# Optimization experiments

Hardware: AMD Instinct MI355X
Metric: run time of the kernel (lower is better)

The kernel has to match this reference:

```python
import jax, jax.numpy as jnp
import numpy as np

D_MODEL = 1024
N_HEADS = 16
HEAD_DIM = D_MODEL // N_HEADS
SEQ_LEN = 2048
BATCH = 4


def setup_inputs() -> dict:
    key = jax.random.key(0)
    k1, k2, k3 = jax.random.split(key, 3)
    x = jax.random.normal(k1, (BATCH, SEQ_LEN, D_MODEL), dtype=jnp.float32)
    # Linear weights stored as [in, out] so y = x @ W (equivalent to torch x @ W.T)
    w_qkv = jax.random.normal(k2, (D_MODEL, 3 * D_MODEL), dtype=jnp.float32) * (D_MODEL ** -0.5)
    w_proj = jax.random.normal(k3, (D_MODEL, D_MODEL), dtype=jnp.float32) * (D_MODEL ** -0.5)
    return {"x": x, "w_qkv": w_qkv, "w_proj": w_proj}


def reference(x, w_qkv, w_proj):
    B, T, C = x.shape
    qkv = x @ w_qkv  # [B, T, 3C]
    q, k, v = jnp.split(qkv, 3, axis=-1)
    # [B, H, T, hd]
    q = q.reshape(B, T, N_HEADS, HEAD_DIM).transpose(0, 2, 1, 3)
    k = k.reshape(B, T, N_HEADS, HEAD_DIM).transpose(0, 2, 1, 3)
    v = v.reshape(B, T, N_HEADS, HEAD_DIM).transpose(0, 2, 1, 3)
    scale = HEAD_DIM ** -0.5
    attn = jnp.einsum("bhqd,bhkd->bhqk", q, k) * scale  # [B, H, T, T]
    causal = jnp.tril(jnp.ones((T, T), dtype=bool))
    attn = jnp.where(causal, attn, -jnp.inf)
    attn = jax.nn.softmax(attn, axis=-1)
    out = jnp.einsum("bhqk,bhkd->bhqd", attn, v)  # [B, H, T, hd]
    out = out.transpose(0, 2, 1, 3).reshape(B, T, C)
    return out @ w_proj
```

## Files before the change

### kernel.cpp

```cpp
#include <hip/hip_runtime.h>
#include <stdint.h>


typedef __bf16 bf16x8 __attribute__((ext_vector_type(8)));
typedef float f32x4 __attribute__((ext_vector_type(4)));
typedef unsigned short u16x8 __attribute__((ext_vector_type(8)));

#define DEVINL static __device__ __forceinline__

DEVINL unsigned short f2b(float f) {
  __bf16 h = (__bf16)f;
  return __builtin_bit_cast(unsigned short, h);
}

DEVINL void gld16(const void* g, void* l) {
  __builtin_amdgcn_global_load_lds(
      (const __attribute__((address_space(1))) void*)g,
      (__attribute__((address_space(3))) void*)l, 16, 0, 0);
}

DEVINL f32x4 mfma16(bf16x8 a, bf16x8 b, f32x4 c) {
  return __builtin_amdgcn_mfma_f32_16x16x32_bf16(a, b, c, 0, 0, 0);
}

#define SCHED_FENCE() __builtin_amdgcn_sched_barrier(0)

__global__ __launch_bounds__(256) void k_cast_bf16(const float* __restrict__ in,
                                                   unsigned short* __restrict__ out,
                                                   int n8) {
  int i = blockIdx.x * 256 + threadIdx.x;
  if (i >= n8) return;
  const float4* p = (const float4*)in + (size_t)i * 2;
  float4 a = p[0], b = p[1];
  u16x8 o;
  o[0] = f2b(a.x); o[1] = f2b(a.y); o[2] = f2b(a.z); o[3] = f2b(a.w);
  o[4] = f2b(b.x); o[5] = f2b(b.y); o[6] = f2b(b.z); o[7] = f2b(b.w);
  *(u16x8*)(out + (size_t)i * 8) = o;
}

__global__ __launch_bounds__(256) void k_transpose_w(const float* __restrict__ in,
                                                     unsigned short* __restrict__ out,
                                                     int R, int C) {
  __shared__ float t[64][65];
  int ci = blockIdx.x * 64, ri = blockIdx.y * 64;
  int tid = threadIdx.x;
#pragma unroll
  for (int j = 0; j < 4; ++j) {
    int c = tid + j * 256;
    int row = c >> 4;
    int col = (c & 15) * 4;
    float4 v = *(const float4*)(in + (size_t)(ri + row) * C + ci + col);
    t[row][col] = v.x; t[row][col + 1] = v.y; t[row][col + 2] = v.z; t[row][col + 3] = v.w;
  }
  __syncthreads();
  int cc = tid >> 2;
  int seg = (tid & 3) * 16;
  u16x8 o0, o1;
#pragma unroll
  for (int j = 0; j < 8; ++j) o0[j] = f2b(t[seg + j][cc]);
#pragma unroll
  for (int j = 0; j < 8; ++j) o1[j] = f2b(t[seg + 8 + j][cc]);
  unsigned short* dst = out + (size_t)(ci + cc) * R + ri + seg;
  *(u16x8*)dst = o0;
  *(u16x8*)(dst + 8) = o1;
}

__global__ __launch_bounds__(256) void k_transpose_v(const unsigned short* __restrict__ v,
                                                     unsigned short* __restrict__ vt) {
  __shared__ unsigned short s[64][65];
  int bh = blockIdx.y;
  int t0 = blockIdx.x * 64;
  int tid = threadIdx.x;
  const unsigned short* src = v + ((size_t)bh * 2048 + t0) * 64;
#pragma unroll
  for (int j = 0; j < 2; ++j) {
    int c = tid + j * 256;
    int row = c >> 3;
    int col = (c & 7) * 8;
    u16x8 x = *(const u16x8*)(src + (size_t)row * 64 + col);
#pragma unroll
    for (int q = 0; q < 8; ++q) s[row][col + q] = x[q];
  }
  __syncthreads();
  int d = tid >> 2;
  int seg = (tid & 3) * 16;
  u16x8 o0, o1;
#pragma unroll
  for (int j = 0; j < 8; ++j) o0[j] = s[seg + j][d];
#pragma unroll
  for (int j = 0; j < 8; ++j) o1[j] = s[seg + 8 + j][d];
  unsigned short* dst = vt + ((size_t)bh * 64 + d) * 2048 + t0 + seg;
  *(u16x8*)dst = o0;
  *(u16x8*)(dst + 8) = o1;
}

template <int MODE>
__global__ __launch_bounds__(256) void k_gemm(const unsigned short* __restrict__ A,
                                              const unsigned short* __restrict__ Bt,
                                              int M, int N, int K,
                                              float* __restrict__ Cf,
                                              unsigned short* __restrict__ qo,
                                              unsigned short* __restrict__ ko,
                                              unsigned short* __restrict__ vo,
                                              float qscale) {
  __shared__ unsigned short As[128 * 32];
  __shared__ unsigned short Bs[128 * 32];
  int tid = threadIdx.x;
  int w = tid >> 6, lane = tid & 63, l15 = lane & 15, l4 = lane >> 4;
  int bn = blockIdx.x, bm = blockIdx.y;
  int wr = (w >> 1) * 64, wc = (w & 1) * 64;
  f32x4 acc[4][4];
#pragma unroll
  for (int i = 0; i < 4; ++i)
#pragma unroll
    for (int j = 0; j < 4; ++j) acc[i][j] = (f32x4){0.f, 0.f, 0.f, 0.f};
  const char* Ab = (const char*)(A + (size_t)bm * 128 * K);
  const char* Bb = (const char*)(Bt + (size_t)bn * 128 * K);
  for (int kt = 0; kt < K; kt += 32) {
#pragma unroll
    for (int c0 = 0; c0 < 2; ++c0) {
      int c = tid + c0 * 256;
      int row = c >> 2, cb = (c & 3) * 16;
      gld16(Ab + ((size_t)row * K + kt) * 2 + cb, (char*)As + c * 16);
      gld16(Bb + ((size_t)row * K + kt) * 2 + cb, (char*)Bs + c * 16);
    }
    __syncthreads();
    bf16x8 af[4], bfr[4];
#pragma unroll
    for (int m = 0; m < 4; ++m)
      af[m] = *(const bf16x8*)((const char*)As + (wr + m * 16 + l15) * 64 + l4 * 16);
#pragma unroll
    for (int n = 0; n < 4; ++n)
      bfr[n] = *(const bf16x8*)((const char*)Bs + (wc + n * 16 + l15) * 64 + l4 * 16);
#pragma unroll
    for (int m = 0; m < 4; ++m)
#pragma unroll
      for (int n = 0; n < 4; ++n)
        acc[m][n] = mfma16(af[m], bfr[n], acc[m][n]);
    __syncthreads();
  }
#pragma unroll
  for (int m = 0; m < 4; ++m) {
    int grow0 = bm * 128 + wr + m * 16 + l4 * 4;
#pragma unroll
    for (int n = 0; n < 4; ++n) {
      int gcol = bn * 128 + wc + n * 16 + l15;
#pragma unroll
      for (int r = 0; r < 4; ++r) {
        int grow = grow0 + r;
        float val = acc[m][n][r];
        if (MODE == 1) {
          Cf[(size_t)grow * N + gcol] = val;
        } else {
          int which = gcol >> 10, rem = gcol & 1023;
          int h = rem >> 6, d = rem & 63;
          int b = grow >> 11, t = grow & 2047;
          size_t off = (((size_t)(b * 16 + h)) * 2048 + t) * 64 + d;
          if (which == 0)      qo[off] = f2b(val * qscale);
          else if (which == 1) ko[off] = f2b(val);
          else                 vo[off] = f2b(val);
        }
      }
    }
  }
}

__global__ __launch_bounds__(256) void k_attn(const unsigned short* __restrict__ Q,
                                              const unsigned short* __restrict__ Kt,
                                              const unsigned short* __restrict__ Vt,
                                              unsigned short* __restrict__ AO) {
  __shared__ unsigned short Ks[2][4096];
  __shared__ unsigned short Vs[2][4096];
  __shared__ unsigned short Ps[4096];
  int tid = threadIdx.x;
  int w = tid >> 6, lane = tid & 63, l15 = lane & 15, l4 = lane >> 4;
  int lin = blockIdx.x;
  int xcd = lin & 7, jj = lin >> 3;
  int bh = xcd * 8 + (jj & 7);
  int p = jj >> 3;
  const char* Kb = (const char*)(Kt + (size_t)bh * 2048 * 64);
  const char* Vb = (const char*)(Vt + (size_t)bh * 64 * 2048);
  const int swp = (l15 & 7) << 4;
  char* Pw = (char*)Ps + w * 2048;
  int b = bh >> 4, h = bh & 15;

  int Lb0 = (w * 64 + lane) * 16;
  int Lb1 = ((w + 4) * 64 + lane) * 16;
  int Nb0 = Lb0 ^ (((Lb0 >> 7) & 7) << 4);
  int Nb1 = Lb1 ^ (((Lb1 >> 7) & 7) << 4);
  int d0 = Nb0 >> 7, in0 = Nb0 & 127;
  int d1 = Nb1 >> 7, in1 = Nb1 & 127;

  auto stage = [&](int t, int buf) {
    size_t kv0 = (size_t)t * 64;
    gld16(Kb + kv0 * 128 + Nb0, (char*)Ks[buf] + Lb0);
    gld16(Vb + (size_t)d0 * 4096 + kv0 * 2 + in0, (char*)Vs[buf] + Lb0);
    gld16(Kb + kv0 * 128 + Nb1, (char*)Ks[buf] + Lb1);
    gld16(Vb + (size_t)d1 * 4096 + kv0 * 2 + in1, (char*)Vs[buf] + Lb1);
  };

  auto run = [&](int qi) {
    int q0 = qi * 64;
    const unsigned short* Qb = Q + ((size_t)bh * 2048 + q0 + w * 16) * 64;
    bf16x8 qf0 = *(const bf16x8*)((const char*)Qb + l15 * 128 + l4 * 16);
    bf16x8 qf1 = *(const bf16x8*)((const char*)Qb + l15 * 128 + 64 + l4 * 16);
    f32x4 o[4];
#pragma unroll
    for (int i = 0; i < 4; ++i) o[i] = (f32x4){0.f, 0.f, 0.f, 0.f};
    float mrow = -1e30f, lrow = 0.f;
    const int ntiles = qi + 1;
    const int qg = w * 16 + l15;
    SCHED_FENCE();
    __builtin_amdgcn_s_barrier();
    SCHED_FENCE();
    stage(0, 0);
    SCHED_FENCE();
    for (int it = 0; it < ntiles; ++it) {
      int cur = it & 1;
      if (it) {
        SCHED_FENCE();
        __builtin_amdgcn_s_barrier();
        SCHED_FENCE();
      }
      if (it + 1 < ntiles) {
        stage(it + 1, cur ^ 1);
        SCHED_FENCE();
        asm volatile("s_waitcnt vmcnt(4)" ::: "memory");
      } else {
        SCHED_FENCE();
        asm volatile("s_waitcnt vmcnt(0)" ::: "memory");
      }
      SCHED_FENCE();
      __builtin_amdgcn_s_barrier();
      SCHED_FENCE();
      const char* Kc = (const char*)Ks[cur];
      const char* Vc = (const char*)Vs[cur];
      f32x4 s[4];
      __builtin_amdgcn_s_setprio(1);
#pragma unroll
      for (int c = 0; c < 4; ++c) {
        int row = c * 16 + l15;
        int base = row * 128 + l4 * 16;
        int sw = (row & 7) << 4;
        bf16x8 k0 = *(const bf16x8*)(Kc + (base ^ sw));
        bf16x8 k1 = *(const bf16x8*)(Kc + ((base + 64) ^ sw));
        f32x4 t = mfma16(k0, qf0, (f32x4){0.f, 0.f, 0.f, 0.f});
        s[c] = mfma16(k1, qf1, t);
      }
      __builtin_amdgcn_s_setprio(0);
      if (it == ntiles - 1) {
#pragma unroll
        for (int c = 0; c < 4; ++c) {
          int kvb = c * 16 + l4 * 4;
#pragma unroll
          for (int r = 0; r < 4; ++r)
            if (kvb + r > qg) s[c][r] = -1e30f;
        }
      }
      float mx = fmaxf(fmaxf(fmaxf(s[0][0], s[0][1]), fmaxf(s[0][2], s[0][3])),
                       fmaxf(fmaxf(s[1][0], s[1][1]), fmaxf(s[1][2], s[1][3])));
      mx = fmaxf(mx, fmaxf(fmaxf(fmaxf(s[2][0], s[2][1]), fmaxf(s[2][2], s[2][3])),
                           fmaxf(fmaxf(s[3][0], s[3][1]), fmaxf(s[3][2], s[3][3]))));
      mx = fmaxf(mx, __shfl_xor(mx, 16));
      mx = fmaxf(mx, __shfl_xor(mx, 32));
      float mn = fmaxf(mrow, mx);
      float corr = __builtin_amdgcn_exp2f(mrow - mn);
      mrow = mn;
      float rs = 0.f;
#pragma unroll
      for (int c = 0; c < 4; ++c) {
        float p0 = __builtin_amdgcn_exp2f(s[c][0] - mn);
        float p1 = __builtin_amdgcn_exp2f(s[c][1] - mn);
        float p2 = __builtin_amdgcn_exp2f(s[c][2] - mn);
        float p3 = __builtin_amdgcn_exp2f(s[c][3] - mn);
        rs += (p0 + p1) + (p2 + p3);
        uint32_t lo = (uint32_t)f2b(p0) | ((uint32_t)f2b(p1) << 16);
        uint32_t hi = (uint32_t)f2b(p2) | ((uint32_t)f2b(p3) << 16);
        *(uint2*)(Pw + ((l15 * 128 + c * 32 + l4 * 8) ^ swp)) = make_uint2(lo, hi);
      }
      rs += __shfl_xor(rs, 16);
      rs += __shfl_xor(rs, 32);
      lrow = lrow * corr + rs;
      float corr_r[4];
#pragma unroll
      for (int r = 0; r < 4; ++r) corr_r[r] = __shfl(corr, l4 * 4 + r);
#pragma unroll
      for (int dc = 0; dc < 4; ++dc)
#pragma unroll
        for (int r = 0; r < 4; ++r) o[dc][r] *= corr_r[r];
      bf16x8 pa[2];
#pragma unroll
      for (int kc = 0; kc < 2; ++kc)
        pa[kc] = *(const bf16x8*)(Pw + ((l15 * 128 + kc * 64 + l4 * 16) ^ swp));
      __builtin_amdgcn_s_setprio(1);
#pragma unroll
      for (int dc = 0; dc < 4; ++dc) {
#pragma unroll
        for (int kc = 0; kc < 2; ++kc) {
          int vrow = dc * 16 + l15;
          int vnat = vrow * 128 + kc * 64 + l4 * 16;
          bf16x8 vb = *(const bf16x8*)(Vc + (vnat ^ ((vrow & 7) << 4)));
          o[dc] = mfma16(pa[kc], vb, o[dc]);
        }
      }
      __builtin_amdgcn_s_setprio(0);
    }
    float inv[4];
#pragma unroll
    for (int r = 0; r < 4; ++r) inv[r] = 1.f / __shfl(lrow, l4 * 4 + r);
#pragma unroll
    for (int dc = 0; dc < 4; ++dc) {
#pragma unroll
      for (int r = 0; r < 4; ++r) {
        int t = q0 + w * 16 + l4 * 4 + r;
        AO[((size_t)(b * 2048 + t)) * 1024 + h * 64 + dc * 16 + l15] =
            f2b(o[dc][r] * inv[r]);
      }
    }
  };

  run(31 - p);
  run(p);
}

extern "C" void kernel_launch(void* const* d_in, const int* in_sizes, int n_in,
                              void* d_out, int out_size, void* d_ws, size_t ws_size,
                              hipStream_t stream) {
  const float* x      = (const float*)d_in[0];
  const float* w_qkv  = (const float*)d_in[1];
  const float* w_proj = (const float*)d_in[2];
  float* out = (float*)d_out;
  char* ws = (char*)d_ws;
  const size_t MB = 1024 * 1024;
  unsigned short* xb     = (unsigned short*)(ws);
  unsigned short* vT     = (unsigned short*)(ws);
  unsigned short* wqkvT  = (unsigned short*)(ws + 16 * MB);
  unsigned short* wprojT = (unsigned short*)(ws + 22 * MB);
  unsigned short* q      = (unsigned short*)(ws + 24 * MB);
  unsigned short* k      = (unsigned short*)(ws + 40 * MB);
  unsigned short* v      = (unsigned short*)(ws + 56 * MB);
  unsigned short* ao     = (unsigned short*)(ws + 56 * MB);

  k_cast_bf16<<<4096, 256, 0, stream>>>(x, xb, 1048576);
  k_transpose_w<<<dim3(48, 16), 256, 0, stream>>>(w_qkv, wqkvT, 1024, 3072);
  k_transpose_w<<<dim3(16, 16), 256, 0, stream>>>(w_proj, wprojT, 1024, 1024);
  const float qscale = 0.125f * 1.44269504088896f;
  k_gemm<0><<<dim3(24, 64), 256, 0, stream>>>(xb, wqkvT, 8192, 3072, 1024,
                                              nullptr, q, k, v, qscale);
  k_transpose_v<<<dim3(32, 64), 256, 0, stream>>>(v, vT);
  k_attn<<<1024, 256, 0, stream>>>(q, k, vT, ao);
  k_gemm<1><<<dim3(8, 64), 256, 0, stream>>>(ao, wprojT, 8192, 1024, 1024,
                                             out, nullptr, nullptr, nullptr, 1.f);
}
```

Measured before the change: 208.3 us.

## Double-buffer GEMM LDS tiles and skip lazy softmax rescaling in attention

The GEMM kernel gets two LDS buffers, so the next K tile is prefetched with global_load_lds while the current one is consumed. It waits with explicit vmcnt counts, uses raw barriers, and raises MFMA priority. The flash-attention loop now rescales the running max, sum and output only when some row's max grows by more than 8 (in log2 units), so most tiles skip the exp, shuffles and multiplies. The cost is twice the GEMM LDS, which may lower occupancy. Probabilities can reach up to 2^8 before rescaling, a small risk to bf16 precision.

```diff
diff --git a/kernel.cpp b/kernel.cpp
--- a/kernel.cpp
+++ b/kernel.cpp
@@ -103,8 +103,8 @@
                                               unsigned short* __restrict__ ko,
                                               unsigned short* __restrict__ vo,
                                               float qscale) {
-  __shared__ unsigned short As[128 * 32];
-  __shared__ unsigned short Bs[128 * 32];
+  __shared__ unsigned short As[2][128 * 32];
+  __shared__ unsigned short Bs[2][128 * 32];
   int tid = threadIdx.x;
   int w = tid >> 6, lane = tid & 63, l15 = lane & 15, l4 = lane >> 4;
   int bn = blockIdx.x, bm = blockIdx.y;
@@ -116,28 +116,54 @@
     for (int j = 0; j < 4; ++j) acc[i][j] = (f32x4){0.f, 0.f, 0.f, 0.f};
   const char* Ab = (const char*)(A + (size_t)bm * 128 * K);
   const char* Bb = (const char*)(Bt + (size_t)bn * 128 * K);
-  for (int kt = 0; kt < K; kt += 32) {
-#pragma unroll
-    for (int c0 = 0; c0 < 2; ++c0) {
-      int c = tid + c0 * 256;
-      int row = c >> 2, cb = (c & 3) * 16;
-      gld16(Ab + ((size_t)row * K + kt) * 2 + cb, (char*)As + c * 16);
-      gld16(Bb + ((size_t)row * K + kt) * 2 + cb, (char*)Bs + c * 16);
-    }
-    __syncthreads();
+  int c_0 = tid, c_1 = tid + 256;
+  int row0 = c_0 >> 2, cb0 = (c_0 & 3) * 16;
+  int row1 = c_1 >> 2, cb1 = (c_1 & 3) * 16;
+
+  auto stage = [&](int kt, int buf) {
+    gld16(Ab + ((size_t)row0 * K + kt) * 2 + cb0, (char*)As[buf] + c_0 * 16);
+    gld16(Bb + ((size_t)row0 * K + kt) * 2 + cb0, (char*)Bs[buf] + c_0 * 16);
+    gld16(Ab + ((size_t)row1 * K + kt) * 2 + cb1, (char*)As[buf] + c_1 * 16);
+    gld16(Bb + ((size_t)row1 * K + kt) * 2 + cb1, (char*)Bs[buf] + c_1 * 16);
+  };
+
+  const int nkt = K >> 5;
+  stage(0, 0);
+  SCHED_FENCE();
+  for (int t = 0; t < nkt; ++t) {
+    int cur = t & 1;
+    if (t) {
+      SCHED_FENCE();
+      __builtin_amdgcn_s_barrier();
+      SCHED_FENCE();
+    }
+    if (t + 1 < nkt) {
+      stage((t + 1) * 32, cur ^ 1);
+      SCHED_FENCE();
+      asm volatile("s_waitcnt vmcnt(4)" ::: "memory");
+    } else {
+      SCHED_FENCE();
+      asm volatile("s_waitcnt vmcnt(0)" ::: "memory");
+    }
+    SCHED_FENCE();
+    __builtin_amdgcn_s_barrier();
+    SCHED_FENCE();
+    const char* Ac = (const char*)As[cur];
+    const char* Bc = (const char*)Bs[cur];
     bf16x8 af[4], bfr[4];
 #pragma unroll
     for (int m = 0; m < 4; ++m)
-      af[m] = *(const bf16x8*)((const char*)As + (wr + m * 16 + l15) * 64 + l4 * 16);
+      af[m] = *(const bf16x8*)(Ac + (wr + m * 16 + l15) * 64 + l4 * 16);
 #pragma unroll
     for (int n = 0; n < 4; ++n)
-      bfr[n] = *(const bf16x8*)((const char*)Bs + (wc + n * 16 + l15) * 64 + l4 * 16);
+      bfr[n] = *(const bf16x8*)(Bc + (wc + n * 16 + l15) * 64 + l4 * 16);
+    __builtin_amdgcn_s_setprio(1);
 #pragma unroll
     for (int m = 0; m < 4; ++m)
 #pragma unroll
       for (int n = 0; n < 4; ++n)
         acc[m][n] = mfma16(af[m], bfr[n], acc[m][n]);
-    __syncthreads();
+    __builtin_amdgcn_s_setprio(0);
   }
 #pragma unroll
   for (int m = 0; m < 4; ++m) {
@@ -263,16 +289,26 @@
                            fmaxf(fmaxf(s[3][0], s[3][1]), fmaxf(s[3][2], s[3][3]))));
       mx = fmaxf(mx, __shfl_xor(mx, 16));
       mx = fmaxf(mx, __shfl_xor(mx, 32));
-      float mn = fmaxf(mrow, mx);
-      float corr = __builtin_amdgcn_exp2f(mrow - mn);
-      mrow = mn;
+      if (!__all(mx - mrow <= 8.f)) {
+        float mn = fmaxf(mrow, mx);
+        float corr = __builtin_amdgcn_exp2f(mrow - mn);
+        mrow = mn;
+        lrow *= corr;
+        float corr_r[4];
+#pragma unroll
+        for (int r = 0; r < 4; ++r) corr_r[r] = __shfl(corr, l4 * 4 + r);
+#pragma unroll
+        for (int dc = 0; dc < 4; ++dc)
+#pragma unroll
+          for (int r = 0; r < 4; ++r) o[dc][r] *= corr_r[r];
+      }
       float rs = 0.f;
 #pragma unroll
       for (int c = 0; c < 4; ++c) {
-        float p0 = __builtin_amdgcn_exp2f(s[c][0] - mn);
-        float p1 = __builtin_amdgcn_exp2f(s[c][1] - mn);
-        float p2 = __builtin_amdgcn_exp2f(s[c][2] - mn);
-        float p3 = __builtin_amdgcn_exp2f(s[c][3] - mn);
+        float p0 = __builtin_amdgcn_exp2f(s[c][0] - mrow);
+        float p1 = __builtin_amdgcn_exp2f(s[c][1] - mrow);
+        float p2 = __builtin_amdgcn_exp2f(s[c][2] - mrow);
+        float p3 = __builtin_amdgcn_exp2f(s[c][3] - mrow);
         rs += (p0 + p1) + (p2 + p3);
         uint32_t lo = (uint32_t)f2b(p0) | ((uint32_t)f2b(p1) << 16);
         uint32_t hi = (uint32_t)f2b(p2) | ((uint32_t)f2b(p3) << 16);
@@ -280,14 +316,7 @@
       }
       rs += __shfl_xor(rs, 16);
       rs += __shfl_xor(rs, 32);
-      lrow = lrow * corr + rs;
-      float corr_r[4];
-#pragma unroll
-      for (int r = 0; r < 4; ++r) corr_r[r] = __shfl(corr, l4 * 4 + r);
-#pragma unroll
-      for (int dc = 0; dc < 4; ++dc)
-#pragma unroll
-        for (int r = 0; r < 4; ++r) o[dc][r] *= corr_r[r];
+      lrow += rs;
       bf16x8 pa[2];
 #pragma unroll
       for (int kc = 0; kc < 2; ++kc)
```

Result: slower. 212.8 us (+2.2%).
